# Optimization experiments

Hardware: AMD Instinct MI355X
Metric: run time of the kernel (lower is better)

Reference implementation:

```python
import jax, jax.numpy as jnp
import numpy as np


def _mlp(params, xin):
    # xin: [..., D] masked spin configuration; returns L2-row-normalized [..., 2]
    W1, b1, W2, b2 = params
    h = jnp.tanh(xin @ W1.T + b1)          # [..., H]
    out = h @ W2.T + b2                     # [..., 2]
    # F.normalize(out, p=2, dim=1)
    return out / jnp.linalg.norm(out, axis=-1, keepdims=True)


def setup_inputs() -> dict:
    key = jax.random.key(0)
    D, H = 64, 256
    k1, k2, k3, k4 = jax.random.split(key, 4)
    s1 = 1.0 / np.sqrt(D)
    s2 = 1.0 / np.sqrt(H)
    return {
        "W1": jax.random.normal(k1, (H, D), jnp.float32) * s1,
        "b1": jax.random.normal(k2, (H,), jnp.float32) * s1,
        "W2": jax.random.normal(k3, (2, H), jnp.float32) * s2,
        "b2": jax.random.normal(k4, (2,), jnp.float32) * s2,
        "N_samples": 2048,
    }


def reference(W1, b1, W2, b2, N_samples):
    params = (W1, b1, W2, b2)
    D = W1.shape[1]
    idx = jnp.arange(D)

    def step(carry, d):
        x, WAV, key = carry
        key, sub = jax.random.split(key)
        mask = (idx < d).astype(x.dtype)                 # growing causal mask [D]
        out = _mlp(params, x * mask)                     # [N, 2]
        psi_pos, psi_neg = out[:, 0], out[:, 1]
        bit = jax.random.bernoulli(sub, jnp.clip(psi_pos ** 2, 0.0, 1.0))
        spin = jnp.where(bit, 1.0, -1.0)                 # 0 -> -1 remap
        x = x.at[:, d].set(spin)
        sel = jnp.where(spin > 0, psi_pos, psi_neg)
        return (x, WAV * sel, key), None

    x0 = jnp.zeros((N_samples, D), jnp.float32)
    w0 = jnp.ones((N_samples,), jnp.float32)
    (x, WAV, _), _ = jax.lax.scan(step, (x0, w0, jax.random.key(1)), idx)

    # ---- per-sample per-parameter gradients of log|psi| ----
    # grads_per_param[p][s] = sum_d grad(psi_sel_d)[s] / psi_sel_d[s]
    #                       = grad_params sum_d log|psi_sel_d(x_s)|
    masks = (idx[None, :] < idx[:, None]).astype(jnp.float32)  # [D, D] strict lower

    def logpsi(p, xr):
        out = _mlp(p, xr[None, :] * masks)               # [D, 2]
        sel = jnp.where(xr > 0, out[:, 0], out[:, 1])    # [D]
        return jnp.sum(jnp.log(jnp.abs(sel)))

    gW1, gb1, gW2, gb2 = jax.vmap(lambda xr: jax.grad(logpsi)(params, xr))(x)
    return WAV, x, gW1, gb1, gW2, gb2
```

## Files before the change

kernel.cpp:

```cpp
#include <hip/hip_runtime.h>
#include <hip/hip_bf16.h>
#include <stdint.h>
#include <math.h>

#define NS 2048
#define DD 64
#define HH 256

#define XO_OFF  ((size_t)NS)
#define GW1_OFF (XO_OFF + (size_t)NS * DD)
#define GB1_OFF (GW1_OFF + (size_t)NS * HH * DD)
#define GW2_OFF (GB1_OFF + (size_t)NS * HH)
#define GB2_OFF (GW2_OFF + (size_t)NS * 2 * HH)

struct SubKeys { uint32_t a[DD]; uint32_t b[DD]; };

__host__ __device__ static inline void tf2x32(uint32_t k0, uint32_t k1,
                                              uint32_t x0, uint32_t x1,
                                              uint32_t* o0, uint32_t* o1) {
  uint32_t ks0 = k0, ks1 = k1, ks2 = k0 ^ k1 ^ 0x1BD11BDAu;
  x0 += ks0; x1 += ks1;
#define TFROT(r) { x0 += x1; x1 = (x1 << (r)) | (x1 >> (32 - (r))); x1 ^= x0; }
  TFROT(13) TFROT(15) TFROT(26) TFROT(6)  x0 += ks1; x1 += ks2 + 1u;
  TFROT(17) TFROT(29) TFROT(16) TFROT(24) x0 += ks2; x1 += ks0 + 2u;
  TFROT(13) TFROT(15) TFROT(26) TFROT(6)  x0 += ks0; x1 += ks1 + 3u;
  TFROT(17) TFROT(29) TFROT(16) TFROT(24) x0 += ks1; x1 += ks2 + 4u;
  TFROT(13) TFROT(15) TFROT(26) TFROT(6)  x0 += ks2; x1 += ks0 + 5u;
#undef TFROT
  *o0 = x0; *o1 = x1;
}

__device__ static inline float fast_tanh(float x) {
  float t = __builtin_amdgcn_exp2f(x * 2.88539008177792681472f);
  return 1.0f - 2.0f / (t + 1.0f);
}

__device__ static inline float fast_tanh_g(float x) {
  float t = __builtin_amdgcn_exp2f(x * 2.88539008177792681472f);
  return 1.0f - 2.0f * __builtin_amdgcn_rcpf(t + 1.0f);
}

__device__ static inline float wave_red_dpp(float x) {
#define DPPADD(ctrl) \
  x += __int_as_float(__builtin_amdgcn_update_dpp(0, __float_as_int(x), (ctrl), 0xf, 0xf, true))
  DPPADD(0x111);
  DPPADD(0x112);
  DPPADD(0x114);
  DPPADD(0x118);
  DPPADD(0x142);
  DPPADD(0x143);
#undef DPPADD
  return __int_as_float(__builtin_amdgcn_readlane(__float_as_int(x), 63));
}

__launch_bounds__(256)
__global__ void QNADE_w1t_kernel(const float* __restrict__ W1,
                                 float* __restrict__ W1T,
                                 float* __restrict__ W1Q) {
  int idx = blockIdx.x * 256 + threadIdx.x;
  int h = idx >> 6, d = idx & 63;
  float v = W1[idx];
  W1T[d * 256 + h] = v;
  W1Q[d * 256 + (h & 63) * 4 + (h >> 6)] = v;
}

__launch_bounds__(256, 8)
__global__ void QNADE_fused_kernel(const float* __restrict__ W1T,
                                   const float* __restrict__ W1Q,
                                   const float* __restrict__ b1,
                                   const float* __restrict__ W2,
                                   const float* __restrict__ b2,
                                   float* __restrict__ out,
                                   SubKeys sk) {
  __shared__ float xrL[DD];
  __shared__ float dzL[2 * DD];
  __shared__ float gbL[HH];
  __shared__ float tbuf[4][16][66];

  const int i    = blockIdx.x;
  const int tid  = threadIdx.x;
  const int lane = tid & 63;
  const int wv   = tid >> 6;
  const int sw   = i & 3;

  const float w20h = W2[tid];
  const float w21h = W2[HH + tid];
  const float b1h  = b1[tid];

  if (wv == sw) {
    uint32_t o0, o1;
    tf2x32(sk.a[lane], sk.b[lane], 0u, (uint32_t)i, &o0, &o1);
    const float u_reg = __uint_as_float(0x3f800000u | ((o0 ^ o1) >> 9)) - 1.0f;

    float z1[4], w20f[4], w21f[4];
    float gw20[4] = {0,0,0,0}, gw21[4] = {0,0,0,0}, gb1a[4] = {0,0,0,0};
    #pragma unroll
    for (int k = 0; k < 4; ++k) {
      int h = lane + 64 * k;
      z1[k]   = b1[h];
      w20f[k] = W2[h];
      w21f[k] = W2[HH + h];
    }
    const float b20 = b2[0], b21 = b2[1];
    float wav = 1.0f, gb20 = 0.0f, gb21 = 0.0f;
    unsigned long long smask = 0ull;

    #pragma unroll 2
    for (int d = 0; d < DD; ++d) {
      const float4 w4 = *(const float4*)&W1Q[d * 256 + lane * 4];

      float hf[4]; float p0 = 0.0f, p1 = 0.0f;
      #pragma unroll
      for (int k = 0; k < 4; ++k) {
        hf[k] = fast_tanh(z1[k]);
        p0 = fmaf(hf[k], w20f[k], p0);
        p1 = fmaf(hf[k], w21f[k], p1);
      }
      float s0 = wave_red_dpp(p0) + b20;
      float s1 = wave_red_dpp(p1) + b21;

      float nrmf = sqrtf(s0 * s0 + s1 * s1);
      float psip = s0 / nrmf;
      float p    = fminf(psip * psip, 1.0f);
      unsigned long long bal = __ballot(u_reg < p);
      bool  bit  = (bal >> d) & 1ull;
      float spinf = bit ? 1.0f : -1.0f;
      if (bit) smask |= (1ull << d);

      float rn   = __builtin_amdgcn_rcpf(nrmf);
      float psin = s1 * rn;
      float self = bit ? psip : psin;
      wav *= self;
      float gf   = __builtin_amdgcn_rcpf(self);
      float dz20 = ((bit ? gf : 0.0f) - psip) * rn;
      float dz21 = ((bit ? 0.0f : gf) - psin) * rn;
      gb20 += dz20; gb21 += dz21;

      #pragma unroll
      for (int k = 0; k < 4; ++k) {
        gw20[k] = fmaf(dz20, hf[k], gw20[k]);
        gw21[k] = fmaf(dz21, hf[k], gw21[k]);
        float dz1k = (dz20 * w20f[k] + dz21 * w21f[k]) * (1.0f - hf[k] * hf[k]);
        gb1a[k] += dz1k;
        float wk = (k == 0) ? w4.x : (k == 1) ? w4.y : (k == 2) ? w4.z : w4.w;
        z1[k] = fmaf(spinf, wk, z1[k]);
      }

      if (lane == 0) { xrL[d] = spinf; dzL[d] = dz20; dzL[DD + d] = dz21; }
    }

    out[XO_OFF + (size_t)i * DD + lane] = ((smask >> lane) & 1ull) ? 1.0f : -1.0f;
    #pragma unroll
    for (int k = 0; k < 4; ++k) {
      int h = lane + 64 * k;
      gbL[h] = gb1a[k];
      out[GW2_OFF + (size_t)i * 2 * HH + h]      = gw20[k];
      out[GW2_OFF + (size_t)i * 2 * HH + HH + h] = gw21[k];
      out[GB1_OFF + (size_t)i * HH + h]          = gb1a[k];
    }
    if (lane == 0) {
      out[i] = wav;
      out[GB2_OFF + (size_t)i * 2 + 0] = gb20;
      out[GB2_OFF + (size_t)i * 2 + 1] = gb21;
    }
  }
  __syncthreads();

  const size_t gw1base = GW1_OFF + (size_t)i * (HH * DD);
  const float gb1f = gbL[tid];
  float z1f = b1h;
  float pref = 0.0f;
  const int q = lane & 3, rr = lane >> 2;

  #pragma unroll
  for (int c = 0; c < 4; ++c) {
    #pragma unroll
    for (int r = 0; r < 16; ++r) {
      const int j = 16 * c + r;
      float hf  = fast_tanh_g(z1f);
      float dz1 = (dzL[j] * w20h + dzL[DD + j] * w21h) * (1.0f - hf * hf);
      pref += dz1;
      float xv = xrL[j];
      tbuf[wv][r][lane] = xv * (gb1f - pref);
      z1f = fmaf(xv, W1T[j * 256 + tid], z1f);
    }
    __syncthreads();
    #pragma unroll
    for (int p2 = 0; p2 < 4; ++p2) {
      const int hp = 16 * p2 + rr;
      float4 v;
      v.x = tbuf[wv][4 * q + 0][hp];
      v.y = tbuf[wv][4 * q + 1][hp];
      v.z = tbuf[wv][4 * q + 2][hp];
      v.w = tbuf[wv][4 * q + 3][hp];
      *(float4*)&out[gw1base + (size_t)(64 * wv + hp) * DD + 16 * c + 4 * q] = v;
    }
    __syncthreads();
  }
}

extern "C" void kernel_launch(void* const* d_in, const int* in_sizes, int n_in,
                              void* d_out, int out_size, void* d_ws, size_t ws_size,
                              hipStream_t stream) {
  (void)in_sizes; (void)n_in; (void)out_size; (void)ws_size;
  const float* W1 = (const float*)d_in[0];
  const float* b1 = (const float*)d_in[1];
  const float* W2 = (const float*)d_in[2];
  const float* b2 = (const float*)d_in[3];
  float* out = (float*)d_out;
  float* W1T = (float*)d_ws;
  float* W1Q = (float*)d_ws + HH * DD;

  SubKeys sk;
  uint32_t k0 = 0u, k1 = 1u;
  for (int d = 0; d < DD; ++d) {
    uint32_t n0, n1, s0, s1;
    tf2x32(k0, k1, 0u, 0u, &n0, &n1);
    tf2x32(k0, k1, 0u, 1u, &s0, &s1);
    sk.a[d] = s0; sk.b[d] = s1;
    k0 = n0; k1 = n1;
  }

  QNADE_w1t_kernel<<<dim3(64), dim3(256), 0, stream>>>(W1, W1T, W1Q);
  QNADE_fused_kernel<<<dim3(NS), dim3(256), 0, stream>>>(W1T, W1Q, b1, W2, b2, out, sk);
}
```

Measured before the change: 72.29 us.

## Move gradient accumulation out of serial sampling wave into reverse-order parallel pass

The single sampling wave no longer accumulates gW2 and gb1 per step. Instead it saves its final pre-activations to shared memory, and all 256 threads replay the dimensions in reverse, undoing each spin's contribution to recover the hidden state. During this replay they accumulate suffix sums for the gW1 and gb1 terms and the gW2 sums. This shortens the serial critical path executed by one wave, while the parallel phase does a little more work. Reconstructing z by subtraction can introduce small floating-point drift.

```diff
diff --git a/kernel.cpp b/kernel.cpp
--- a/kernel.cpp
+++ b/kernel.cpp
@@ -30,11 +30,6 @@
   *o0 = x0; *o1 = x1;
 }
 
-__device__ static inline float fast_tanh(float x) {
-  float t = __builtin_amdgcn_exp2f(x * 2.88539008177792681472f);
-  return 1.0f - 2.0f / (t + 1.0f);
-}
-
 __device__ static inline float fast_tanh_g(float x) {
   float t = __builtin_amdgcn_exp2f(x * 2.88539008177792681472f);
   return 1.0f - 2.0f * __builtin_amdgcn_rcpf(t + 1.0f);
@@ -74,7 +69,7 @@
                                    SubKeys sk) {
   __shared__ float xrL[DD];
   __shared__ float dzL[2 * DD];
-  __shared__ float gbL[HH];
+  __shared__ float zfL[HH];
   __shared__ float tbuf[4][16][66];
 
   const int i    = blockIdx.x;
@@ -85,7 +80,6 @@
 
   const float w20h = W2[tid];
   const float w21h = W2[HH + tid];
-  const float b1h  = b1[tid];
 
   if (wv == sw) {
     uint32_t o0, o1;
@@ -93,7 +87,6 @@
     const float u_reg = __uint_as_float(0x3f800000u | ((o0 ^ o1) >> 9)) - 1.0f;
 
     float z1[4], w20f[4], w21f[4];
-    float gw20[4] = {0,0,0,0}, gw21[4] = {0,0,0,0}, gb1a[4] = {0,0,0,0};
     #pragma unroll
     for (int k = 0; k < 4; ++k) {
       int h = lane + 64 * k;
@@ -112,7 +105,7 @@
       float hf[4]; float p0 = 0.0f, p1 = 0.0f;
       #pragma unroll
       for (int k = 0; k < 4; ++k) {
-        hf[k] = fast_tanh(z1[k]);
+        hf[k] = fast_tanh_g(z1[k]);
         p0 = fmaf(hf[k], w20f[k], p0);
         p1 = fmaf(hf[k], w21f[k], p1);
       }
@@ -138,10 +131,6 @@
 
       #pragma unroll
       for (int k = 0; k < 4; ++k) {
-        gw20[k] = fmaf(dz20, hf[k], gw20[k]);
-        gw21[k] = fmaf(dz21, hf[k], gw21[k]);
-        float dz1k = (dz20 * w20f[k] + dz21 * w21f[k]) * (1.0f - hf[k] * hf[k]);
-        gb1a[k] += dz1k;
         float wk = (k == 0) ? w4.x : (k == 1) ? w4.y : (k == 2) ? w4.z : w4.w;
         z1[k] = fmaf(spinf, wk, z1[k]);
       }
@@ -149,15 +138,9 @@
       if (lane == 0) { xrL[d] = spinf; dzL[d] = dz20; dzL[DD + d] = dz21; }
     }
 
+    #pragma unroll
+    for (int k = 0; k < 4; ++k) zfL[lane + 64 * k] = z1[k];
     out[XO_OFF + (size_t)i * DD + lane] = ((smask >> lane) & 1ull) ? 1.0f : -1.0f;
-    #pragma unroll
-    for (int k = 0; k < 4; ++k) {
-      int h = lane + 64 * k;
-      gbL[h] = gb1a[k];
-      out[GW2_OFF + (size_t)i * 2 * HH + h]      = gw20[k];
-      out[GW2_OFF + (size_t)i * 2 * HH + HH + h] = gw21[k];
-      out[GB1_OFF + (size_t)i * HH + h]          = gb1a[k];
-    }
     if (lane == 0) {
       out[i] = wav;
       out[GB2_OFF + (size_t)i * 2 + 0] = gb20;
@@ -167,22 +150,25 @@
   __syncthreads();
 
   const size_t gw1base = GW1_OFF + (size_t)i * (HH * DD);
-  const float gb1f = gbL[tid];
-  float z1f = b1h;
-  float pref = 0.0f;
+  float z1b  = zfL[tid];
+  float suf  = 0.0f;
+  float gw20 = 0.0f, gw21 = 0.0f;
   const int q = lane & 3, rr = lane >> 2;
 
   #pragma unroll
-  for (int c = 0; c < 4; ++c) {
-    #pragma unroll
-    for (int r = 0; r < 16; ++r) {
+  for (int c = 3; c >= 0; --c) {
+    #pragma unroll
+    for (int r = 15; r >= 0; --r) {
       const int j = 16 * c + r;
-      float hf  = fast_tanh_g(z1f);
-      float dz1 = (dzL[j] * w20h + dzL[DD + j] * w21h) * (1.0f - hf * hf);
-      pref += dz1;
-      float xv = xrL[j];
-      tbuf[wv][r][lane] = xv * (gb1f - pref);
-      z1f = fmaf(xv, W1T[j * 256 + tid], z1f);
+      const float xv = xrL[j];
+      z1b = fmaf(-xv, W1T[j * 256 + tid], z1b);
+      float hf  = fast_tanh_g(z1b);
+      float d0  = dzL[j], d1 = dzL[DD + j];
+      float dz1 = (d0 * w20h + d1 * w21h) * (1.0f - hf * hf);
+      tbuf[wv][r][lane] = xv * suf;
+      suf  += dz1;
+      gw20  = fmaf(d0, hf, gw20);
+      gw21  = fmaf(d1, hf, gw21);
     }
     __syncthreads();
     #pragma unroll
@@ -197,6 +183,10 @@
     }
     __syncthreads();
   }
+
+  out[GB1_OFF + (size_t)i * HH + tid]          = suf;
+  out[GW2_OFF + (size_t)i * 2 * HH + tid]      = gw20;
+  out[GW2_OFF + (size_t)i * 2 * HH + HH + tid] = gw21;
 }
 
 extern "C" void kernel_launch(void* const* d_in, const int* in_sizes, int n_in,
```

Result: slower. 80.42 us (+11.2%).

## Spread autoregressive sampling across all four waves with shared-memory cross-wave reduction

Applied to the files above, without the earlier changes.

Before, the 64-step sampling loop ran on a single wave per block, with each lane handling four hidden units while the other three waves sat idle. Now every thread owns one hidden unit, and the per-wave DPP partial sums are combined through a double-buffered shared array. That needs one __syncthreads per step. The change cuts per-wave serial work by four, but adds 64 block-level barriers and an LDS round trip on the critical path. It also drops the W1Q layout buffer that the old kernel needed.

```diff
diff --git a/kernel.cpp b/kernel.cpp
--- a/kernel.cpp
+++ b/kernel.cpp
@@ -54,19 +54,14 @@
 }
 
 __launch_bounds__(256)
-__global__ void QNADE_w1t_kernel(const float* __restrict__ W1,
-                                 float* __restrict__ W1T,
-                                 float* __restrict__ W1Q) {
+__global__ void QNADE_w1t_kernel(const float* __restrict__ W1, float* __restrict__ W1T) {
   int idx = blockIdx.x * 256 + threadIdx.x;
   int h = idx >> 6, d = idx & 63;
-  float v = W1[idx];
-  W1T[d * 256 + h] = v;
-  W1Q[d * 256 + (h & 63) * 4 + (h >> 6)] = v;
+  W1T[d * 256 + h] = W1[idx];
 }
 
 __launch_bounds__(256, 8)
 __global__ void QNADE_fused_kernel(const float* __restrict__ W1T,
-                                   const float* __restrict__ W1Q,
                                    const float* __restrict__ b1,
                                    const float* __restrict__ W2,
                                    const float* __restrict__ b2,
@@ -75,94 +70,79 @@
   __shared__ float xrL[DD];
   __shared__ float dzL[2 * DD];
   __shared__ float gbL[HH];
+  __shared__ float pex[2][4][2];
   __shared__ float tbuf[4][16][66];
 
   const int i    = blockIdx.x;
   const int tid  = threadIdx.x;
   const int lane = tid & 63;
   const int wv   = tid >> 6;
-  const int sw   = i & 3;
-
-  const float w20h = W2[tid];
-  const float w21h = W2[HH + tid];
-  const float b1h  = b1[tid];
-
-  if (wv == sw) {
-    uint32_t o0, o1;
-    tf2x32(sk.a[lane], sk.b[lane], 0u, (uint32_t)i, &o0, &o1);
-    const float u_reg = __uint_as_float(0x3f800000u | ((o0 ^ o1) >> 9)) - 1.0f;
-
-    float z1[4], w20f[4], w21f[4];
-    float gw20[4] = {0,0,0,0}, gw21[4] = {0,0,0,0}, gb1a[4] = {0,0,0,0};
-    #pragma unroll
-    for (int k = 0; k < 4; ++k) {
-      int h = lane + 64 * k;
-      z1[k]   = b1[h];
-      w20f[k] = W2[h];
-      w21f[k] = W2[HH + h];
-    }
-    const float b20 = b2[0], b21 = b2[1];
-    float wav = 1.0f, gb20 = 0.0f, gb21 = 0.0f;
-    unsigned long long smask = 0ull;
-
-    #pragma unroll 2
-    for (int d = 0; d < DD; ++d) {
-      const float4 w4 = *(const float4*)&W1Q[d * 256 + lane * 4];
-
-      float hf[4]; float p0 = 0.0f, p1 = 0.0f;
-      #pragma unroll
-      for (int k = 0; k < 4; ++k) {
-        hf[k] = fast_tanh(z1[k]);
-        p0 = fmaf(hf[k], w20f[k], p0);
-        p1 = fmaf(hf[k], w21f[k], p1);
-      }
-      float s0 = wave_red_dpp(p0) + b20;
-      float s1 = wave_red_dpp(p1) + b21;
-
-      float nrmf = sqrtf(s0 * s0 + s1 * s1);
-      float psip = s0 / nrmf;
-      float p    = fminf(psip * psip, 1.0f);
-      unsigned long long bal = __ballot(u_reg < p);
-      bool  bit  = (bal >> d) & 1ull;
-      float spinf = bit ? 1.0f : -1.0f;
-      if (bit) smask |= (1ull << d);
-
-      float rn   = __builtin_amdgcn_rcpf(nrmf);
-      float psin = s1 * rn;
-      float self = bit ? psip : psin;
-      wav *= self;
-      float gf   = __builtin_amdgcn_rcpf(self);
-      float dz20 = ((bit ? gf : 0.0f) - psip) * rn;
-      float dz21 = ((bit ? 0.0f : gf) - psin) * rn;
-      gb20 += dz20; gb21 += dz21;
-
-      #pragma unroll
-      for (int k = 0; k < 4; ++k) {
-        gw20[k] = fmaf(dz20, hf[k], gw20[k]);
-        gw21[k] = fmaf(dz21, hf[k], gw21[k]);
-        float dz1k = (dz20 * w20f[k] + dz21 * w21f[k]) * (1.0f - hf[k] * hf[k]);
-        gb1a[k] += dz1k;
-        float wk = (k == 0) ? w4.x : (k == 1) ? w4.y : (k == 2) ? w4.z : w4.w;
-        z1[k] = fmaf(spinf, wk, z1[k]);
-      }
-
-      if (lane == 0) { xrL[d] = spinf; dzL[d] = dz20; dzL[DD + d] = dz21; }
-    }
-
-    out[XO_OFF + (size_t)i * DD + lane] = ((smask >> lane) & 1ull) ? 1.0f : -1.0f;
-    #pragma unroll
-    for (int k = 0; k < 4; ++k) {
-      int h = lane + 64 * k;
-      gbL[h] = gb1a[k];
-      out[GW2_OFF + (size_t)i * 2 * HH + h]      = gw20[k];
-      out[GW2_OFF + (size_t)i * 2 * HH + HH + h] = gw21[k];
-      out[GB1_OFF + (size_t)i * HH + h]          = gb1a[k];
-    }
-    if (lane == 0) {
-      out[i] = wav;
-      out[GB2_OFF + (size_t)i * 2 + 0] = gb20;
-      out[GB2_OFF + (size_t)i * 2 + 1] = gb21;
-    }
+
+  uint32_t o0, o1;
+  tf2x32(sk.a[lane], sk.b[lane], 0u, (uint32_t)i, &o0, &o1);
+  const float u_reg = __uint_as_float(0x3f800000u | ((o0 ^ o1) >> 9)) - 1.0f;
+
+  const float w20 = W2[tid];
+  const float w21 = W2[HH + tid];
+  const float b1h = b1[tid];
+  const float b20 = b2[0], b21 = b2[1];
+
+  float z1 = b1h;
+  float wav = 1.0f, gb20 = 0.0f, gb21 = 0.0f;
+  float gw20 = 0.0f, gw21 = 0.0f, gb1a = 0.0f;
+  unsigned long long smask = 0ull;
+
+  #pragma unroll 2
+  for (int d = 0; d < DD; ++d) {
+    const float wq = W1T[d * 256 + tid];
+
+    float hf = fast_tanh(z1);
+    float r0 = wave_red_dpp(hf * w20);
+    float r1 = wave_red_dpp(hf * w21);
+    const int par = d & 1;
+    if (lane == 0) { pex[par][wv][0] = r0; pex[par][wv][1] = r1; }
+    __syncthreads();
+    float s0 = ((pex[par][0][0] + pex[par][1][0]) +
+                (pex[par][2][0] + pex[par][3][0])) + b20;
+    float s1 = ((pex[par][0][1] + pex[par][1][1]) +
+                (pex[par][2][1] + pex[par][3][1])) + b21;
+
+    float nrmf = sqrtf(s0 * s0 + s1 * s1);
+    float psip = s0 / nrmf;
+    float p    = fminf(psip * psip, 1.0f);
+    unsigned long long bal = __ballot(u_reg < p);
+    bool  bit  = (bal >> d) & 1ull;
+    float spinf = bit ? 1.0f : -1.0f;
+    if (bit) smask |= (1ull << d);
+
+    float rn   = __builtin_amdgcn_rcpf(nrmf);
+    float psin = s1 * rn;
+    float self = bit ? psip : psin;
+    wav *= self;
+    float gf   = __builtin_amdgcn_rcpf(self);
+    float dz20 = ((bit ? gf : 0.0f) - psip) * rn;
+    float dz21 = ((bit ? 0.0f : gf) - psin) * rn;
+    gb20 += dz20; gb21 += dz21;
+
+    gw20 = fmaf(dz20, hf, gw20);
+    gw21 = fmaf(dz21, hf, gw21);
+    float dz1k = (dz20 * w20 + dz21 * w21) * (1.0f - hf * hf);
+    gb1a += dz1k;
+    z1 = fmaf(spinf, wq, z1);
+
+    if (tid == 0) { xrL[d] = spinf; dzL[d] = dz20; dzL[DD + d] = dz21; }
+  }
+
+  gbL[tid] = gb1a;
+  out[GB1_OFF + (size_t)i * HH + tid]          = gb1a;
+  out[GW2_OFF + (size_t)i * 2 * HH + tid]      = gw20;
+  out[GW2_OFF + (size_t)i * 2 * HH + HH + tid] = gw21;
+  if (wv == 0) out[XO_OFF + (size_t)i * DD + lane] =
+      ((smask >> lane) & 1ull) ? 1.0f : -1.0f;
+  if (tid == 0) {
+    out[i] = wav;
+    out[GB2_OFF + (size_t)i * 2 + 0] = gb20;
+    out[GB2_OFF + (size_t)i * 2 + 1] = gb21;
   }
   __syncthreads();
 
@@ -178,7 +158,7 @@
     for (int r = 0; r < 16; ++r) {
       const int j = 16 * c + r;
       float hf  = fast_tanh_g(z1f);
-      float dz1 = (dzL[j] * w20h + dzL[DD + j] * w21h) * (1.0f - hf * hf);
+      float dz1 = (dzL[j] * w20 + dzL[DD + j] * w21) * (1.0f - hf * hf);
       pref += dz1;
       float xv = xrL[j];
       tbuf[wv][r][lane] = xv * (gb1f - pref);
@@ -209,7 +189,6 @@
   const float* b2 = (const float*)d_in[3];
   float* out = (float*)d_out;
   float* W1T = (float*)d_ws;
-  float* W1Q = (float*)d_ws + HH * DD;
 
   SubKeys sk;
   uint32_t k0 = 0u, k1 = 1u;
@@ -221,6 +200,6 @@
     k0 = n0; k1 = n1;
   }
 
-  QNADE_w1t_kernel<<<dim3(64), dim3(256), 0, stream>>>(W1, W1T, W1Q);
-  QNADE_fused_kernel<<<dim3(NS), dim3(256), 0, stream>>>(W1T, W1Q, b1, W2, b2, out, sk);
-}
+  QNADE_w1t_kernel<<<dim3(64), dim3(256), 0, stream>>>(W1, W1T);
+  QNADE_fused_kernel<<<dim3(NS), dim3(256), 0, stream>>>(W1T, b1, W2, b2, out, sk);
+}
```

Result: slower. 110.1 us (+52.3%).
